# Performance work log

Measured on AMD Instinct MI355X. Metric: run time of the kernel, lower is better.

## Reference

```python
import jax, jax.numpy as jnp
import numpy as np


def _conv1x1(x, w, b=None):
    # x: [B, Cin, N, S], w: [Cout, Cin], 1x1 Conv2d
    y = jnp.einsum('oc,bcns->bons', w, x)
    if b is not None:
        y = y + b[None, :, None, None]
    return y


def setup_inputs() -> dict:
    key = jax.random.key(0)
    ks = jax.random.split(key, 16)
    B, Cin, N, K = 4, 128, 16384, 16
    MID, OUT, SHARE, PT = 64, 128, 8, 10
    s = 0.05
    inp = {
        'sm_feats': jax.random.normal(ks[0], (B, Cin, N, K), jnp.float32),
        'sm_ppfs': jax.random.normal(ks[1], (B, PT, N, K), jnp.float32),
        'conv0_w': jax.random.normal(ks[2], (OUT, Cin), jnp.float32) * s,
        'conv0_b': jax.random.normal(ks[3], (OUT,), jnp.float32) * s,
        'conv1_w': jax.random.normal(ks[4], (MID, OUT), jnp.float32) * s,
        'conv1_b': jax.random.normal(ks[5], (MID,), jnp.float32) * s,
        'conv2_w': jax.random.normal(ks[6], (MID, OUT), jnp.float32) * s,
        'conv2_b': jax.random.normal(ks[7], (MID,), jnp.float32) * s,
        'conv3_w': jax.random.normal(ks[8], (MID, OUT), jnp.float32) * s,
        'conv3_b': jax.random.normal(ks[9], (MID,), jnp.float32) * s,
        'convw1_w': jax.random.normal(ks[10], (MID // SHARE, MID * K), jnp.float32) * s,
        'convw2_w': jax.random.normal(ks[11], (K * MID // SHARE, MID // SHARE), jnp.float32) * s,
        'convw2_b': jax.random.normal(ks[12], (K * MID // SHARE,), jnp.float32) * s,
        'convout_w': jax.random.normal(ks[13], (OUT, MID), jnp.float32) * s,
        'convout_b': jax.random.normal(ks[14], (OUT,), jnp.float32) * s,
        'pt1_w': jax.random.normal(ks[15], (MID, PT), jnp.float32) * s,
        'pt2_w': jax.random.normal(jax.random.fold_in(key, 99), (MID, MID), jnp.float32) * s,
    }
    return inp


def reference(sm_feats, sm_ppfs, conv0_w, conv0_b, conv1_w, conv1_b, conv2_w, conv2_b,
              conv3_w, conv3_b, convw1_w, convw2_w, convw2_b, convout_w, convout_b,
              pt1_w, pt2_w):
    xn = jax.nn.relu(_conv1x1(sm_feats, conv0_w, conv0_b))  # [B, OUT, N, K]
    x = xn[..., :1]                                          # center point feature
    identity = x
    x1 = _conv1x1(x, conv1_w, conv1_b)       # [B, MID, N, 1]
    x2 = _conv1x1(xn, conv2_w, conv2_b)      # [B, MID, N, K]
    x3 = _conv1x1(xn, conv3_w, conv3_b)      # [B, MID, N, K]
    ptf = _conv1x1(jax.nn.relu(_conv1x1(sm_ppfs, pt1_w)), pt2_w)  # [B, MID, N, K]
    x3 = x3 + ptf
    xfs = x1 - x2 + ptf                      # [B, MID, N, K]
    B, MID, N, K = xfs.shape
    share = MID // convw1_w.shape[0]
    xfs = jnp.transpose(xfs, (0, 1, 3, 2)).reshape(B, MID * K, 1, N)
    h = jax.nn.relu(_conv1x1(xfs, convw1_w))            # [B, MID//share, 1, N]
    w = _conv1x1(h, convw2_w, convw2_b)                  # [B, K*MID//share, 1, N]
    w = jax.nn.softmax(w.reshape(B, MID // share, K, N), axis=2)
    w = jnp.transpose(w, (0, 1, 3, 2))                   # [B, MID//share, N, K]
    w = jnp.tile(w, (1, share, 1, 1))                    # [B, MID, N, K]
    out = jax.nn.relu(jnp.sum(w * x3, axis=3, keepdims=True))  # [B, MID, N, 1]
    out = (_conv1x1(out, convout_w, convout_b) + identity).squeeze(3)  # [B, OUT, N]
    return out
```

## Files before the change

kernel.cpp:

```cpp
#include <hip/hip_runtime.h>
#include <hip/hip_bf16.h>


typedef __attribute__((ext_vector_type(8))) short bf16x8;
typedef __attribute__((ext_vector_type(4))) float f32x4;
typedef __attribute__((ext_vector_type(4))) unsigned short us4;

#define MFMA(a, b, c) __builtin_amdgcn_mfma_f32_16x16x32_bf16((a), (b), (c), 0, 0, 0)

#define OFF_F    0
#define OFF_X2   0
#define OFF_PTF  17408
#define OFF_XN   34816
#define OFF_X3   34816
#define OFF_XFS  52224
#define OFF_P    69632
#define OFF_WS   69632
#define OFF_HB   74752
#define OFF_OM   76288
#define OFF_X1   77824
#define OFF_XC   78912
#define SMEM_BYTES 81088

#define WS_W0  0
#define WS_W1  16384
#define WS_W2  24576
#define WS_W3  32768
#define WS_P1  40960
#define WS_P2  43008
#define WS_CW1 47104
#define WS_WO  63488
#define WS_TOTAL 71680

__device__ __forceinline__ unsigned short f2b(float f) {
    union { __hip_bfloat16 h; unsigned short u; } v;
    v.h = __float2bfloat16(f);
    return v.u;
}
__device__ __forceinline__ float b2f(unsigned short u) {
    union { unsigned u; float f; } v;
    v.u = ((unsigned)u) << 16;
    return v.f;
}
__device__ __forceinline__ us4 pk4(float a, float b, float c, float d) {
    us4 r; r[0] = f2b(a); r[1] = f2b(b); r[2] = f2b(c); r[3] = f2b(d); return r;
}
__device__ __forceinline__ bf16x8 ldb(const unsigned short* p) {
    return *(const bf16x8*)p;
}

__global__ __launch_bounds__(512, 1)
void convert_weights(const float* __restrict__ w0, const float* __restrict__ w1,
                     const float* __restrict__ w2, const float* __restrict__ w3,
                     const float* __restrict__ p1, const float* __restrict__ p2,
                     const float* __restrict__ cw1, const float* __restrict__ wo,
                     unsigned short* __restrict__ ws) {
    int i = blockIdx.x * 512 + threadIdx.x;
    if (i >= WS_TOTAL) return;
    float v;
    if (i < 16384)      v = w0[i];
    else if (i < 24576) v = w1[i - 16384];
    else if (i < 32768) v = w2[i - 24576];
    else if (i < 40960) v = w3[i - 32768];
    else if (i < 43008) { int r = i - 40960, row = r >> 5, k = r & 31;
                          v = (k < 10) ? p1[row * 10 + k] : 0.f; }
    else if (i < 47104) v = p2[i - 43008];
    else if (i < 63488) { int r = i - 47104, j = r >> 10, kc = r & 1023;
                          v = (j < 8) ? cw1[j * 1024 + (kc & 63) * 16 + (kc >> 6)] : 0.f; }
    else                v = wo[i - 63488];
    ws[i] = f2b(v);
}

__global__ __launch_bounds__(512, 4)
void fused_model_kernel(const float* __restrict__ feats, const float* __restrict__ ppfs,
                        const unsigned short* __restrict__ wsb,
                        const float* __restrict__ b0, const float* __restrict__ b1,
                        const float* __restrict__ b2, const float* __restrict__ b3,
                        const float* __restrict__ cw2, const float* __restrict__ cb2,
                        const float* __restrict__ bo, float* __restrict__ out) {
    extern __shared__ char smem[];
    const int tid = threadIdx.x;
    const int W = tid >> 6;
    const int lane = tid & 63;
    const int kk = lane & 15;
    const int g = lane >> 4;
    const int bid = blockIdx.x;
    const int b = bid >> 11;
    const int n0 = (bid & 2047) * 8;

    bf16x8 a0[4], rA[4], rB[4];
    {
        const int mtr = (W & 3);
        #pragma unroll
        for (int kt = 0; kt < 4; ++kt) {
            a0[kt] = ldb(wsb + WS_W0 + (16 * W + kk) * 128 + kt * 32 + 8 * g);
            if (W < 4) {
                rA[kt] = ldb(wsb + WS_W3 + (16 * mtr + kk) * 128 + kt * 32 + 8 * g);
                rB[kt] = ldb(wsb + WS_W1 + (16 * mtr + kk) * 128 + kt * 32 + 8 * g);
            } else {
                rA[kt] = ldb(wsb + WS_W2 + (16 * mtr + kk) * 128 + kt * 32 + 8 * g);
                rB[kt] = ldb(wsb + WS_W3 + (16 * mtr + kk) * 128 + kt * 32 + 8 * g);
            }
        }
    }

    {
        const int kq = tid & 3, ci = tid >> 2;
        const int cisw = (ci * 2) ^ (kq << 4);
        #pragma unroll
        for (int pos = 0; pos < 8; ++pos) {
            f32x4 v = *(const f32x4*)(feats + (((size_t)b * 128 + ci) * 16384 + (n0 + pos)) * 16 + kq * 4);
            char* base = smem + OFF_F + pos * 4352 + cisw;
            *(unsigned short*)(base + (kq * 4 + 0) * 272) = f2b(v[0]);
            *(unsigned short*)(base + (kq * 4 + 1) * 272) = f2b(v[1]);
            *(unsigned short*)(base + (kq * 4 + 2) * 272) = f2b(v[2]);
            *(unsigned short*)(base + (kq * 4 + 3) * 272) = f2b(v[3]);
        }
        if (tid < 320) {
            int pos = tid / 40, r = tid % 40, p = r >> 2, kq2 = r & 3;
            f32x4 v = *(const f32x4*)(ppfs + (((size_t)b * 10 + p) * 16384 + (n0 + pos)) * 16 + kq2 * 4);
            char* base = smem + OFF_P + pos * 1024 + p * 2;
            *(unsigned short*)(base + (kq2 * 4 + 0) * 64) = f2b(v[0]);
            *(unsigned short*)(base + (kq2 * 4 + 1) * 64) = f2b(v[1]);
            *(unsigned short*)(base + (kq2 * 4 + 2) * 64) = f2b(v[2]);
            *(unsigned short*)(base + (kq2 * 4 + 3) * 64) = f2b(v[3]);
        } else {
            for (int z = tid - 320; z < 1408; z += 192) {
                int pos = z / 176, rr = z % 176, ks = rr / 11, dw = rr % 11;
                *(unsigned*)(smem + OFF_P + pos * 1024 + ks * 64 + 20 + dw * 4) = 0u;
            }
        }
    }
    __syncthreads();

    {
        f32x4 bv = *(const f32x4*)(b0 + 16 * W + 4 * g);
        const int fsw = ((kk >> 2) & 3) << 4;
        #pragma unroll
        for (int pos = 0; pos < 8; ++pos) {
            f32x4 acc = {0.f, 0.f, 0.f, 0.f};
            #pragma unroll
            for (int kt = 0; kt < 4; ++kt) {
                bf16x8 bf = *(const bf16x8*)(smem + OFF_F + pos * 4352 + kk * 272 + ((kt * 64 + 16 * g) ^ fsw));
                acc = MFMA(a0[kt], bf, acc);
            }
            us4 xw = pk4(fmaxf(acc[0] + bv[0], 0.f), fmaxf(acc[1] + bv[1], 0.f),
                         fmaxf(acc[2] + bv[2], 0.f), fmaxf(acc[3] + bv[3], 0.f));
            *(us4*)(smem + OFF_XN + pos * 4352 + kk * 272 + (16 * W + 4 * g) * 2) = xw;
            if (kk == 0) *(us4*)(smem + OFF_XC + pos * 272 + (16 * W + 4 * g) * 2) = xw;
        }
    }
    __syncthreads();

    f32x4 acc3[4];
    if (W < 4) {
        bf16x8 a1[4], a2[4][2];
        #pragma unroll
        for (int mt = 0; mt < 4; ++mt) {
            a1[mt] = ldb(wsb + WS_P1 + (16 * mt + kk) * 32 + 8 * g);
            a2[mt][0] = ldb(wsb + WS_P2 + (16 * mt + kk) * 64 + 8 * g);
            a2[mt][1] = ldb(wsb + WS_P2 + (16 * mt + kk) * 64 + 32 + 8 * g);
        }
        const int sel = g >> 1;
        const int sa = kk + 16 * ((2 * g) & 3);
        const int sb = kk + 16 * ((2 * g + 1) & 3);
        #pragma unroll
        for (int pp = 0; pp < 2; ++pp) {
            const int pos = 2 * W + pp;
            bf16x8 bp = *(const bf16x8*)(smem + OFF_P + pos * 1024 + kk * 64 + 16 * g);
            int pkd[4][2];
            #pragma unroll
            for (int mt = 0; mt < 4; ++mt) {
                f32x4 hv = {0.f, 0.f, 0.f, 0.f};
                hv = MFMA(a1[mt], bp, hv);
                us4 t = pk4(fmaxf(hv[0], 0.f), fmaxf(hv[1], 0.f),
                            fmaxf(hv[2], 0.f), fmaxf(hv[3], 0.f));
                pkd[mt][0] = ((int*)&t)[0];
                pkd[mt][1] = ((int*)&t)[1];
            }
            union { int d[4]; bf16x8 v; } bh0, bh1;
            bh0.d[0] = sel ? __shfl(pkd[1][0], sa, 64) : __shfl(pkd[0][0], sa, 64);
            bh0.d[1] = sel ? __shfl(pkd[1][1], sa, 64) : __shfl(pkd[0][1], sa, 64);
            bh0.d[2] = sel ? __shfl(pkd[1][0], sb, 64) : __shfl(pkd[0][0], sb, 64);
            bh0.d[3] = sel ? __shfl(pkd[1][1], sb, 64) : __shfl(pkd[0][1], sb, 64);
            bh1.d[0] = sel ? __shfl(pkd[3][0], sa, 64) : __shfl(pkd[2][0], sa, 64);
            bh1.d[1] = sel ? __shfl(pkd[3][1], sa, 64) : __shfl(pkd[2][1], sa, 64);
            bh1.d[2] = sel ? __shfl(pkd[3][0], sb, 64) : __shfl(pkd[2][0], sb, 64);
            bh1.d[3] = sel ? __shfl(pkd[3][1], sb, 64) : __shfl(pkd[2][1], sb, 64);
            #pragma unroll
            for (int mt = 0; mt < 4; ++mt) {
                f32x4 acc = {0.f, 0.f, 0.f, 0.f};
                acc = MFMA(a2[mt][0], bh0.v, acc);
                acc = MFMA(a2[mt][1], bh1.v, acc);
                *(us4*)(smem + OFF_PTF + pos * 2176 + kk * 136 + (16 * mt + 4 * g) * 2) =
                    pk4(acc[0], acc[1], acc[2], acc[3]);
            }
        }
        #pragma unroll
        for (int pp = 0; pp < 4; ++pp) {
            f32x4 acc = {0.f, 0.f, 0.f, 0.f};
            #pragma unroll
            for (int kt = 0; kt < 4; ++kt) {
                bf16x8 bf = *(const bf16x8*)(smem + OFF_XN + pp * 4352 + kk * 272 + (kt * 64 + 16 * g));
                acc = MFMA(rA[kt], bf, acc);
            }
            acc3[pp] = acc;
        }
        f32x4 a1c = {0.f, 0.f, 0.f, 0.f};
        #pragma unroll
        for (int kt = 0; kt < 4; ++kt) {
            bf16x8 bf = *(const bf16x8*)(smem + OFF_XC + (kk & 7) * 272 + (kt * 64 + 16 * g));
            a1c = MFMA(rB[kt], bf, a1c);
        }
        if (kk < 8) {
            f32x4 b1v = *(const f32x4*)(b1 + 16 * W + 4 * g);
            *(us4*)(smem + OFF_X1 + kk * 136 + (16 * W + 4 * g) * 2) =
                pk4(a1c[0] + b1v[0], a1c[1] + b1v[1], a1c[2] + b1v[2], a1c[3] + b1v[3]);
        }
    } else {
        const int mt = W - 4;
        f32x4 b2v = *(const f32x4*)(b2 + 16 * mt + 4 * g);
        #pragma unroll
        for (int pos = 0; pos < 8; ++pos) {
            bf16x8 bx[4];
            #pragma unroll
            for (int kt = 0; kt < 4; ++kt)
                bx[kt] = *(const bf16x8*)(smem + OFF_XN + pos * 4352 + kk * 272 + (kt * 64 + 16 * g));
            f32x4 acc = {0.f, 0.f, 0.f, 0.f};
            #pragma unroll
            for (int kt = 0; kt < 4; ++kt) acc = MFMA(rA[kt], bx[kt], acc);
            *(us4*)(smem + OFF_X2 + pos * 2176 + kk * 136 + (16 * mt + 4 * g) * 2) =
                pk4(acc[0] + b2v[0], acc[1] + b2v[1], acc[2] + b2v[2], acc[3] + b2v[3]);
            if (pos >= 4) {
                f32x4 c = {0.f, 0.f, 0.f, 0.f};
                #pragma unroll
                for (int kt = 0; kt < 4; ++kt) c = MFMA(rB[kt], bx[kt], c);
                acc3[pos - 4] = c;
            }
        }
    }
    __syncthreads();

    {
        const int mt = W & 3, ph = W >> 2;
        f32x4 b3v = *(const f32x4*)(b3 + 16 * mt + 4 * g);
        const int rot = (32 * mt + 8 * g + 16 * kk) & 127;
        #pragma unroll
        for (int pp = 0; pp < 4; ++pp) {
            const int pos = ph * 4 + pp;
            us4 ptfv = *(const us4*)(smem + OFF_PTF + pos * 2176 + kk * 136 + (16 * mt + 4 * g) * 2);
            us4 x2v  = *(const us4*)(smem + OFF_X2  + pos * 2176 + kk * 136 + (16 * mt + 4 * g) * 2);
            us4 x1v  = *(const us4*)(smem + OFF_X1  + pos * 136 + (16 * mt + 4 * g) * 2);
            float pf0 = b2f(ptfv[0]), pf1 = b2f(ptfv[1]), pf2 = b2f(ptfv[2]), pf3 = b2f(ptfv[3]);
            *(us4*)(smem + OFF_X3 + pos * 2176 + kk * 136 + (16 * mt + 4 * g) * 2) =
                pk4(acc3[pp][0] + b3v[0] + pf0, acc3[pp][1] + b3v[1] + pf1,
                    acc3[pp][2] + b3v[2] + pf2, acc3[pp][3] + b3v[3] + pf3);
            *(us4*)(smem + OFF_XFS + pos * 2080 + kk * 128 + rot) =
                pk4(b2f(x1v[0]) - b2f(x2v[0]) + pf0, b2f(x1v[1]) - b2f(x2v[1]) + pf1,
                    b2f(x1v[2]) - b2f(x2v[2]) + pf2, b2f(x1v[3]) - b2f(x2v[3]) + pf3);
        }
        if (tid < 64) *(float*)(smem + OFF_HB + tid * 4) = 0.f;
    }
    __syncthreads();

    {
        bf16x8 acw[4];
        #pragma unroll
        for (int kt = 0; kt < 4; ++kt)
            acw[kt] = ldb(wsb + WS_CW1 + kk * 1024 + W * 128 + kt * 32 + 8 * g);
        const char* xb = smem + OFF_XFS + (kk & 7) * 2080;
        f32x4 acc = {0.f, 0.f, 0.f, 0.f};
        #pragma unroll
        for (int kt = 0; kt < 4; ++kt) {
            const int k = 2 * W + (kt >> 1);
            const int byt = (64 * (kt & 1) + 16 * g + 16 * k) & 127;
            bf16x8 bf = *(const bf16x8*)(xb + k * 128 + byt);
            acc = MFMA(acw[kt], bf, acc);
        }
        if (kk < 8 && g < 2) {
            #pragma unroll
            for (int r = 0; r < 4; ++r)
                atomicAdd((float*)(smem + OFF_HB + kk * 32 + (4 * g + r) * 4), acc[r]);
        }
    }
    __syncthreads();

    {
        const int pos = W;
        f32x4 h0 = *(const f32x4*)(smem + OFF_HB + pos * 32);
        f32x4 h1 = *(const f32x4*)(smem + OFF_HB + pos * 32 + 16);
        #pragma unroll
        for (int r = 0; r < 4; ++r) { h0[r] = fmaxf(h0[r], 0.f); h1[r] = fmaxf(h1[r], 0.f); }
        #pragma unroll
        for (int it = 0; it < 2; ++it) {
            const int c = it * 64 + lane;
            float wl = cb2[c];
            f32x4 w20 = *(const f32x4*)(cw2 + c * 8);
            f32x4 w21 = *(const f32x4*)(cw2 + c * 8 + 4);
            #pragma unroll
            for (int j = 0; j < 4; ++j) {
                wl += w20[j] * h0[j];
                wl += w21[j] * h1[j];
            }
            float mx = wl;
            for (int off = 8; off; off >>= 1) mx = fmaxf(mx, __shfl_xor(mx, off, 16));
            float e = __expf(wl - mx);
            float ss = e;
            for (int off = 8; off; off >>= 1) ss += __shfl_xor(ss, off, 16);
            *(float*)(smem + OFF_WS + pos * 640 + (4 * it + g) * 80 + kk * 4) = e / ss;
        }
        __builtin_amdgcn_wave_barrier();
        __builtin_amdgcn_sched_barrier(0);

        const char* wsp = smem + OFF_WS + pos * 640 + (lane & 7) * 80;
        f32x4 wv0 = *(const f32x4*)(wsp);
        f32x4 wv1 = *(const f32x4*)(wsp + 16);
        f32x4 wv2 = *(const f32x4*)(wsp + 32);
        f32x4 wv3 = *(const f32x4*)(wsp + 48);
        const char* x3b = smem + OFF_X3 + pos * 2176 + lane * 2;
        float s = 0.f;
        #pragma unroll
        for (int k = 0; k < 4; ++k) s += wv0[k] * b2f(*(const unsigned short*)(x3b + k * 136));
        #pragma unroll
        for (int k = 0; k < 4; ++k) s += wv1[k] * b2f(*(const unsigned short*)(x3b + (k + 4) * 136));
        #pragma unroll
        for (int k = 0; k < 4; ++k) s += wv2[k] * b2f(*(const unsigned short*)(x3b + (k + 8) * 136));
        #pragma unroll
        for (int k = 0; k < 4; ++k) s += wv3[k] * b2f(*(const unsigned short*)(x3b + (k + 12) * 136));
        *(unsigned short*)(smem + OFF_OM + pos * 144 + lane * 2) = f2b(fmaxf(s, 0.f));
    }
    __syncthreads();

    {
        f32x4 acc = {0.f, 0.f, 0.f, 0.f};
        #pragma unroll
        for (int kt = 0; kt < 2; ++kt) {
            bf16x8 bf = *(const bf16x8*)(smem + OFF_OM + (kk & 7) * 144 + (kt * 64 + 16 * g));
            acc = MFMA(ldb(wsb + WS_WO + (16 * W + kk) * 64 + kt * 32 + 8 * g), bf, acc);
        }
        if (kk < 8) {
            f32x4 bv = *(const f32x4*)(bo + 16 * W + 4 * g);
            us4 xcv = *(const us4*)(smem + OFF_XC + kk * 272 + (16 * W + 4 * g) * 2);
            #pragma unroll
            for (int r = 0; r < 4; ++r) {
                int o = 16 * W + 4 * g + r;
                out[((size_t)b * 128 + o) * 16384 + n0 + kk] = acc[r] + bv[r] + b2f(xcv[r]);
            }
        }
    }
}

extern "C" void kernel_launch(void* const* d_in, const int* in_sizes, int n_in,
                              void* d_out, int out_size, void* d_ws, size_t ws_size,
                              hipStream_t stream) {
    (void)in_sizes; (void)n_in; (void)out_size; (void)ws_size;
    const float* feats = (const float*)d_in[0];
    const float* ppfs  = (const float*)d_in[1];
    const float* w0  = (const float*)d_in[2];
    const float* b0  = (const float*)d_in[3];
    const float* w1  = (const float*)d_in[4];
    const float* b1  = (const float*)d_in[5];
    const float* w2  = (const float*)d_in[6];
    const float* b2  = (const float*)d_in[7];
    const float* w3  = (const float*)d_in[8];
    const float* b3  = (const float*)d_in[9];
    const float* cw1 = (const float*)d_in[10];
    const float* cw2 = (const float*)d_in[11];
    const float* cb2 = (const float*)d_in[12];
    const float* wo  = (const float*)d_in[13];
    const float* bo  = (const float*)d_in[14];
    const float* p1  = (const float*)d_in[15];
    const float* p2  = (const float*)d_in[16];
    float* out = (float*)d_out;
    unsigned short* wsb = (unsigned short*)d_ws;

    convert_weights<<<dim3((WS_TOTAL + 511) / 512), dim3(512), 0, stream>>>(
        w0, w1, w2, w3, p1, p2, cw1, wo, wsb);

    (void)hipFuncSetAttribute(reinterpret_cast<const void*>(fused_model_kernel),
                              hipFuncAttributeMaxDynamicSharedMemorySize, SMEM_BYTES);
    fused_model_kernel<<<dim3(8192), dim3(512), SMEM_BYTES, stream>>>(
        feats, ppfs, wsb, b0, b1, b2, b3, cw2, cb2, bo, out);
}
```

Before: 303.6 us.

## Halve points per block to shrink LDS and raise occupancy

Each block now processes 4 points instead of 8, which halves the shared-memory footprint (about 41KB instead of 81KB) and doubles the grid. Launch bounds go from 4 to 6 blocks per CU so more blocks can stay resident and hide global-load latency. Work is remapped to the 8 waves: each of the first four waves handles one point in the ppf stage, and the softmax-weighted sum is split across wave halves. Per-block fixed costs, such as loading weight fragments into registers and the several barriers, are now spread over fewer points, and the tighter register budget could cause spills.

```diff
diff --git a/kernel.cpp b/kernel.cpp
--- a/kernel.cpp
+++ b/kernel.cpp
@@ -10,17 +10,17 @@
 
 #define OFF_F    0
 #define OFF_X2   0
-#define OFF_PTF  17408
-#define OFF_XN   34816
-#define OFF_X3   34816
-#define OFF_XFS  52224
-#define OFF_P    69632
-#define OFF_WS   69632
-#define OFF_HB   74752
-#define OFF_OM   76288
-#define OFF_X1   77824
-#define OFF_XC   78912
-#define SMEM_BYTES 81088
+#define OFF_PTF  8704
+#define OFF_XN   17408
+#define OFF_X3   17408
+#define OFF_XFS  26112
+#define OFF_P    34816
+#define OFF_WS   34816
+#define OFF_HB   38912
+#define OFF_OM   39040
+#define OFF_X1   39616
+#define OFF_XC   40160
+#define SMEM_BYTES 41344
 
 #define WS_W0  0
 #define WS_W1  16384
@@ -71,7 +71,7 @@
     ws[i] = f2b(v);
 }
 
-__global__ __launch_bounds__(512, 4)
+__global__ __launch_bounds__(512, 6)
 void fused_model_kernel(const float* __restrict__ feats, const float* __restrict__ ppfs,
                         const unsigned short* __restrict__ wsb,
                         const float* __restrict__ b0, const float* __restrict__ b1,
@@ -85,8 +85,8 @@
     const int kk = lane & 15;
     const int g = lane >> 4;
     const int bid = blockIdx.x;
-    const int b = bid >> 11;
-    const int n0 = (bid & 2047) * 8;
+    const int b = bid >> 12;
+    const int n0 = (bid & 4095) * 4;
 
     bf16x8 a0[4], rA[4], rB[4];
     {
@@ -108,7 +108,7 @@
         const int kq = tid & 3, ci = tid >> 2;
         const int cisw = (ci * 2) ^ (kq << 4);
         #pragma unroll
-        for (int pos = 0; pos < 8; ++pos) {
+        for (int pos = 0; pos < 4; ++pos) {
             f32x4 v = *(const f32x4*)(feats + (((size_t)b * 128 + ci) * 16384 + (n0 + pos)) * 16 + kq * 4);
             char* base = smem + OFF_F + pos * 4352 + cisw;
             *(unsigned short*)(base + (kq * 4 + 0) * 272) = f2b(v[0]);
@@ -116,7 +116,7 @@
             *(unsigned short*)(base + (kq * 4 + 2) * 272) = f2b(v[2]);
             *(unsigned short*)(base + (kq * 4 + 3) * 272) = f2b(v[3]);
         }
-        if (tid < 320) {
+        if (tid < 160) {
             int pos = tid / 40, r = tid % 40, p = r >> 2, kq2 = r & 3;
             f32x4 v = *(const f32x4*)(ppfs + (((size_t)b * 10 + p) * 16384 + (n0 + pos)) * 16 + kq2 * 4);
             char* base = smem + OFF_P + pos * 1024 + p * 2;
@@ -125,7 +125,7 @@
             *(unsigned short*)(base + (kq2 * 4 + 2) * 64) = f2b(v[2]);
             *(unsigned short*)(base + (kq2 * 4 + 3) * 64) = f2b(v[3]);
         } else {
-            for (int z = tid - 320; z < 1408; z += 192) {
+            for (int z = tid - 160; z < 704; z += 352) {
                 int pos = z / 176, rr = z % 176, ks = rr / 11, dw = rr % 11;
                 *(unsigned*)(smem + OFF_P + pos * 1024 + ks * 64 + 20 + dw * 4) = 0u;
             }
@@ -137,7 +137,7 @@
         f32x4 bv = *(const f32x4*)(b0 + 16 * W + 4 * g);
         const int fsw = ((kk >> 2) & 3) << 4;
         #pragma unroll
-        for (int pos = 0; pos < 8; ++pos) {
+        for (int pos = 0; pos < 4; ++pos) {
             f32x4 acc = {0.f, 0.f, 0.f, 0.f};
             #pragma unroll
             for (int kt = 0; kt < 4; ++kt) {
@@ -152,52 +152,42 @@
     }
     __syncthreads();
 
-    f32x4 acc3[4];
+    f32x4 acc3[2];
     if (W < 4) {
-        bf16x8 a1[4], a2[4][2];
+        const int pos = W;
+        bf16x8 bp = *(const bf16x8*)(smem + OFF_P + pos * 1024 + kk * 64 + 16 * g);
+        int pkd[4][2];
         #pragma unroll
         for (int mt = 0; mt < 4; ++mt) {
-            a1[mt] = ldb(wsb + WS_P1 + (16 * mt + kk) * 32 + 8 * g);
-            a2[mt][0] = ldb(wsb + WS_P2 + (16 * mt + kk) * 64 + 8 * g);
-            a2[mt][1] = ldb(wsb + WS_P2 + (16 * mt + kk) * 64 + 32 + 8 * g);
+            bf16x8 a1 = ldb(wsb + WS_P1 + (16 * mt + kk) * 32 + 8 * g);
+            f32x4 hv = {0.f, 0.f, 0.f, 0.f};
+            hv = MFMA(a1, bp, hv);
+            us4 t = pk4(fmaxf(hv[0], 0.f), fmaxf(hv[1], 0.f), fmaxf(hv[2], 0.f), fmaxf(hv[3], 0.f));
+            pkd[mt][0] = ((int*)&t)[0];
+            pkd[mt][1] = ((int*)&t)[1];
         }
         const int sel = g >> 1;
         const int sa = kk + 16 * ((2 * g) & 3);
         const int sb = kk + 16 * ((2 * g + 1) & 3);
+        union { int d[4]; bf16x8 v; } bh0, bh1;
+        bh0.d[0] = sel ? __shfl(pkd[1][0], sa, 64) : __shfl(pkd[0][0], sa, 64);
+        bh0.d[1] = sel ? __shfl(pkd[1][1], sa, 64) : __shfl(pkd[0][1], sa, 64);
+        bh0.d[2] = sel ? __shfl(pkd[1][0], sb, 64) : __shfl(pkd[0][0], sb, 64);
+        bh0.d[3] = sel ? __shfl(pkd[1][1], sb, 64) : __shfl(pkd[0][1], sb, 64);
+        bh1.d[0] = sel ? __shfl(pkd[3][0], sa, 64) : __shfl(pkd[2][0], sa, 64);
+        bh1.d[1] = sel ? __shfl(pkd[3][1], sa, 64) : __shfl(pkd[2][1], sa, 64);
+        bh1.d[2] = sel ? __shfl(pkd[3][0], sb, 64) : __shfl(pkd[2][0], sb, 64);
+        bh1.d[3] = sel ? __shfl(pkd[3][1], sb, 64) : __shfl(pkd[2][1], sb, 64);
+        #pragma unroll
+        for (int mt = 0; mt < 4; ++mt) {
+            f32x4 acc = {0.f, 0.f, 0.f, 0.f};
+            acc = MFMA(ldb(wsb + WS_P2 + (16 * mt + kk) * 64 + 8 * g), bh0.v, acc);
+            acc = MFMA(ldb(wsb + WS_P2 + (16 * mt + kk) * 64 + 32 + 8 * g), bh1.v, acc);
+            *(us4*)(smem + OFF_PTF + pos * 2176 + kk * 136 + (16 * mt + 4 * g) * 2) =
+                pk4(acc[0], acc[1], acc[2], acc[3]);
+        }
         #pragma unroll
         for (int pp = 0; pp < 2; ++pp) {
-            const int pos = 2 * W + pp;
-            bf16x8 bp = *(const bf16x8*)(smem + OFF_P + pos * 1024 + kk * 64 + 16 * g);
-            int pkd[4][2];
-            #pragma unroll
-            for (int mt = 0; mt < 4; ++mt) {
-                f32x4 hv = {0.f, 0.f, 0.f, 0.f};
-                hv = MFMA(a1[mt], bp, hv);
-                us4 t = pk4(fmaxf(hv[0], 0.f), fmaxf(hv[1], 0.f),
-                            fmaxf(hv[2], 0.f), fmaxf(hv[3], 0.f));
-                pkd[mt][0] = ((int*)&t)[0];
-                pkd[mt][1] = ((int*)&t)[1];
-            }
-            union { int d[4]; bf16x8 v; } bh0, bh1;
-            bh0.d[0] = sel ? __shfl(pkd[1][0], sa, 64) : __shfl(pkd[0][0], sa, 64);
-            bh0.d[1] = sel ? __shfl(pkd[1][1], sa, 64) : __shfl(pkd[0][1], sa, 64);
-            bh0.d[2] = sel ? __shfl(pkd[1][0], sb, 64) : __shfl(pkd[0][0], sb, 64);
-            bh0.d[3] = sel ? __shfl(pkd[1][1], sb, 64) : __shfl(pkd[0][1], sb, 64);
-            bh1.d[0] = sel ? __shfl(pkd[3][0], sa, 64) : __shfl(pkd[2][0], sa, 64);
-            bh1.d[1] = sel ? __shfl(pkd[3][1], sa, 64) : __shfl(pkd[2][1], sa, 64);
-            bh1.d[2] = sel ? __shfl(pkd[3][0], sb, 64) : __shfl(pkd[2][0], sb, 64);
-            bh1.d[3] = sel ? __shfl(pkd[3][1], sb, 64) : __shfl(pkd[2][1], sb, 64);
-            #pragma unroll
-            for (int mt = 0; mt < 4; ++mt) {
-                f32x4 acc = {0.f, 0.f, 0.f, 0.f};
-                acc = MFMA(a2[mt][0], bh0.v, acc);
-                acc = MFMA(a2[mt][1], bh1.v, acc);
-                *(us4*)(smem + OFF_PTF + pos * 2176 + kk * 136 + (16 * mt + 4 * g) * 2) =
-                    pk4(acc[0], acc[1], acc[2], acc[3]);
-            }
-        }
-        #pragma unroll
-        for (int pp = 0; pp < 4; ++pp) {
             f32x4 acc = {0.f, 0.f, 0.f, 0.f};
             #pragma unroll
             for (int kt = 0; kt < 4; ++kt) {
@@ -209,10 +199,10 @@
         f32x4 a1c = {0.f, 0.f, 0.f, 0.f};
         #pragma unroll
         for (int kt = 0; kt < 4; ++kt) {
-            bf16x8 bf = *(const bf16x8*)(smem + OFF_XC + (kk & 7) * 272 + (kt * 64 + 16 * g));
+            bf16x8 bf = *(const bf16x8*)(smem + OFF_XC + (kk & 3) * 272 + (kt * 64 + 16 * g));
             a1c = MFMA(rB[kt], bf, a1c);
         }
-        if (kk < 8) {
+        if (kk < 4) {
             f32x4 b1v = *(const f32x4*)(b1 + 16 * W + 4 * g);
             *(us4*)(smem + OFF_X1 + kk * 136 + (16 * W + 4 * g) * 2) =
                 pk4(a1c[0] + b1v[0], a1c[1] + b1v[1], a1c[2] + b1v[2], a1c[3] + b1v[3]);
@@ -221,7 +211,7 @@
         const int mt = W - 4;
         f32x4 b2v = *(const f32x4*)(b2 + 16 * mt + 4 * g);
         #pragma unroll
-        for (int pos = 0; pos < 8; ++pos) {
+        for (int pos = 0; pos < 4; ++pos) {
             bf16x8 bx[4];
             #pragma unroll
             for (int kt = 0; kt < 4; ++kt)
@@ -231,11 +221,11 @@
             for (int kt = 0; kt < 4; ++kt) acc = MFMA(rA[kt], bx[kt], acc);
             *(us4*)(smem + OFF_X2 + pos * 2176 + kk * 136 + (16 * mt + 4 * g) * 2) =
                 pk4(acc[0] + b2v[0], acc[1] + b2v[1], acc[2] + b2v[2], acc[3] + b2v[3]);
-            if (pos >= 4) {
+            if (pos >= 2) {
                 f32x4 c = {0.f, 0.f, 0.f, 0.f};
                 #pragma unroll
                 for (int kt = 0; kt < 4; ++kt) c = MFMA(rB[kt], bx[kt], c);
-                acc3[pos - 4] = c;
+                acc3[pos - 2] = c;
             }
         }
     }
@@ -246,8 +236,8 @@
         f32x4 b3v = *(const f32x4*)(b3 + 16 * mt + 4 * g);
         const int rot = (32 * mt + 8 * g + 16 * kk) & 127;
         #pragma unroll
-        for (int pp = 0; pp < 4; ++pp) {
-            const int pos = ph * 4 + pp;
+        for (int pp = 0; pp < 2; ++pp) {
+            const int pos = ph * 2 + pp;
             us4 ptfv = *(const us4*)(smem + OFF_PTF + pos * 2176 + kk * 136 + (16 * mt + 4 * g) * 2);
             us4 x2v  = *(const us4*)(smem + OFF_X2  + pos * 2176 + kk * 136 + (16 * mt + 4 * g) * 2);
             us4 x1v  = *(const us4*)(smem + OFF_X1  + pos * 136 + (16 * mt + 4 * g) * 2);
@@ -259,7 +249,7 @@
                 pk4(b2f(x1v[0]) - b2f(x2v[0]) + pf0, b2f(x1v[1]) - b2f(x2v[1]) + pf1,
                     b2f(x1v[2]) - b2f(x2v[2]) + pf2, b2f(x1v[3]) - b2f(x2v[3]) + pf3);
         }
-        if (tid < 64) *(float*)(smem + OFF_HB + tid * 4) = 0.f;
+        if (tid < 32) *(float*)(smem + OFF_HB + tid * 4) = 0.f;
     }
     __syncthreads();
 
@@ -268,7 +258,7 @@
         #pragma unroll
         for (int kt = 0; kt < 4; ++kt)
             acw[kt] = ldb(wsb + WS_CW1 + kk * 1024 + W * 128 + kt * 32 + 8 * g);
-        const char* xb = smem + OFF_XFS + (kk & 7) * 2080;
+        const char* xb = smem + OFF_XFS + (kk & 3) * 2080;
         f32x4 acc = {0.f, 0.f, 0.f, 0.f};
         #pragma unroll
         for (int kt = 0; kt < 4; ++kt) {
@@ -277,7 +267,7 @@
             bf16x8 bf = *(const bf16x8*)(xb + k * 128 + byt);
             acc = MFMA(acw[kt], bf, acc);
         }
-        if (kk < 8 && g < 2) {
+        if (kk < 4 && g < 2) {
             #pragma unroll
             for (int r = 0; r < 4; ++r)
                 atomicAdd((float*)(smem + OFF_HB + kk * 32 + (4 * g + r) * 4), acc[r]);
@@ -286,14 +276,13 @@
     __syncthreads();
 
     {
-        const int pos = W;
+        const int pos = W & 3, h = W >> 2;
         f32x4 h0 = *(const f32x4*)(smem + OFF_HB + pos * 32);
         f32x4 h1 = *(const f32x4*)(smem + OFF_HB + pos * 32 + 16);
         #pragma unroll
         for (int r = 0; r < 4; ++r) { h0[r] = fmaxf(h0[r], 0.f); h1[r] = fmaxf(h1[r], 0.f); }
-        #pragma unroll
-        for (int it = 0; it < 2; ++it) {
-            const int c = it * 64 + lane;
+        {
+            const int c = h * 64 + lane;
             float wl = cb2[c];
             f32x4 w20 = *(const f32x4*)(cw2 + c * 8);
             f32x4 w21 = *(const f32x4*)(cw2 + c * 8 + 4);
@@ -307,27 +296,31 @@
             float e = __expf(wl - mx);
             float ss = e;
             for (int off = 8; off; off >>= 1) ss += __shfl_xor(ss, off, 16);
-            *(float*)(smem + OFF_WS + pos * 640 + (4 * it + g) * 80 + kk * 4) = e / ss;
+            *(float*)(smem + OFF_WS + pos * 640 + (4 * h + g) * 80 + kk * 4) = e / ss;
         }
         __builtin_amdgcn_wave_barrier();
         __builtin_amdgcn_sched_barrier(0);
 
-        const char* wsp = smem + OFF_WS + pos * 640 + (lane & 7) * 80;
-        f32x4 wv0 = *(const f32x4*)(wsp);
-        f32x4 wv1 = *(const f32x4*)(wsp + 16);
-        f32x4 wv2 = *(const f32x4*)(wsp + 32);
-        f32x4 wv3 = *(const f32x4*)(wsp + 48);
-        const char* x3b = smem + OFF_X3 + pos * 2176 + lane * 2;
-        float s = 0.f;
-        #pragma unroll
-        for (int k = 0; k < 4; ++k) s += wv0[k] * b2f(*(const unsigned short*)(x3b + k * 136));
-        #pragma unroll
-        for (int k = 0; k < 4; ++k) s += wv1[k] * b2f(*(const unsigned short*)(x3b + (k + 4) * 136));
-        #pragma unroll
-        for (int k = 0; k < 4; ++k) s += wv2[k] * b2f(*(const unsigned short*)(x3b + (k + 8) * 136));
-        #pragma unroll
-        for (int k = 0; k < 4; ++k) s += wv3[k] * b2f(*(const unsigned short*)(x3b + (k + 12) * 136));
-        *(unsigned short*)(smem + OFF_OM + pos * 144 + lane * 2) = f2b(fmaxf(s, 0.f));
+        if (lane < 32) {
+            const int q = lane >> 2, s = lane & 3;
+            const int m = 8 * q + 4 * h + s;
+            const char* wsp = smem + OFF_WS + pos * 640 + (4 * h + s) * 80;
+            f32x4 wv0 = *(const f32x4*)(wsp);
+            f32x4 wv1 = *(const f32x4*)(wsp + 16);
+            f32x4 wv2 = *(const f32x4*)(wsp + 32);
+            f32x4 wv3 = *(const f32x4*)(wsp + 48);
+            const char* x3b = smem + OFF_X3 + pos * 2176 + m * 2;
+            float sacc = 0.f;
+            #pragma unroll
+            for (int k = 0; k < 4; ++k) sacc += wv0[k] * b2f(*(const unsigned short*)(x3b + k * 136));
+            #pragma unroll
+            for (int k = 0; k < 4; ++k) sacc += wv1[k] * b2f(*(const unsigned short*)(x3b + (k + 4) * 136));
+            #pragma unroll
+            for (int k = 0; k < 4; ++k) sacc += wv2[k] * b2f(*(const unsigned short*)(x3b + (k + 8) * 136));
+            #pragma unroll
+            for (int k = 0; k < 4; ++k) sacc += wv3[k] * b2f(*(const unsigned short*)(x3b + (k + 12) * 136));
+            *(unsigned short*)(smem + OFF_OM + pos * 144 + m * 2) = f2b(fmaxf(sacc, 0.f));
+        }
     }
     __syncthreads();
 
@@ -335,10 +328,10 @@
         f32x4 acc = {0.f, 0.f, 0.f, 0.f};
         #pragma unroll
         for (int kt = 0; kt < 2; ++kt) {
-            bf16x8 bf = *(const bf16x8*)(smem + OFF_OM + (kk & 7) * 144 + (kt * 64 + 16 * g));
+            bf16x8 bf = *(const bf16x8*)(smem + OFF_OM + (kk & 3) * 144 + (kt * 64 + 16 * g));
             acc = MFMA(ldb(wsb + WS_WO + (16 * W + kk) * 64 + kt * 32 + 8 * g), bf, acc);
         }
-        if (kk < 8) {
+        if (kk < 4) {
             f32x4 bv = *(const f32x4*)(bo + 16 * W + 4 * g);
             us4 xcv = *(const us4*)(smem + OFF_XC + kk * 272 + (16 * W + 4 * g) * 2);
             #pragma unroll
@@ -377,8 +370,6 @@
     convert_weights<<<dim3((WS_TOTAL + 511) / 512), dim3(512), 0, stream>>>(
         w0, w1, w2, w3, p1, p2, cw1, wo, wsb);
 
-    (void)hipFuncSetAttribute(reinterpret_cast<const void*>(fused_model_kernel),
-                              hipFuncAttributeMaxDynamicSharedMemorySize, SMEM_BYTES);
-    fused_model_kernel<<<dim3(8192), dim3(512), SMEM_BYTES, stream>>>(
+    fused_model_kernel<<<dim3(16384), dim3(512), SMEM_BYTES, stream>>>(
         feats, ppfs, wsb, b0, b1, b2, b3, cw2, cb2, bo, out);
 }
```

After: 494.5 us. 62.9% more time.
